# Performance work log

Hardware: AMD Instinct MI355X
Metric: run time of the kernel (lower is better)

## Reference

```python
import jax, jax.numpy as jnp
import numpy as np

N = 8192          # n_nodes; must equal OUT due to _weight_norm broadcasting
IN = 512          # in_features
OUT = 8192        # out_features
ALPHA = 0.2       # leaky relu negative slope
NEG_INF = -9e15   # mask value used by the torch module


def setup_inputs() -> dict:
    key = jax.random.key(0)
    k1, k2, k3, k4 = jax.random.split(key, 4)
    x = jax.random.normal(k1, (N, IN), jnp.float32)
    adj = jax.random.randint(k2, (N, N), 0, 2, jnp.int32)
    # nn.Linear weight [out_features, in_features]
    W = jax.random.normal(k3, (OUT, IN), jnp.float32) / np.sqrt(IN)
    # attention vector a: [2*out_features, 1], xavier_uniform-ish scale
    a = jax.random.normal(k4, (2 * OUT, 1), jnp.float32) * (1.414 * np.sqrt(2.0 / (2 * OUT + 1)))
    return {"x": x, "adj": adj, "W": W, "a": a}


def reference(x, adj, W, a):
    h = x @ W.T                                   # [N, OUT] (OUT == N)
    # torch._weight_norm(h, g, dim=1) = h * g / ||h||_cols  (norm over dim 0, kept as [1, OUT])
    col_norm = jnp.linalg.norm(h, axis=0, keepdims=True)   # [1, OUT]
    a1 = a[:OUT]                                  # [OUT, 1]
    a2 = a[OUT:]                                  # [OUT, 1]
    wn1 = h * (a1 / col_norm)                     # [N, N]: h[i,j]*a1[i]/norm[j]
    wn2 = h * (a2 / col_norm)                     # [N, N]
    e = jax.nn.leaky_relu(wn1 + wn2.T, ALPHA)     # [N, N]
    scores = jnp.where(adj > 0, e, NEG_INF)
    attention = jax.nn.softmax(scores, axis=1)    # dropout omitted (eval / deterministic)
    return attention @ h                          # [N, OUT]
```

## Files before the change

### kernel.cpp

```cpp
#include <hip/hip_runtime.h>
#include <hip/hip_bf16.h>
#include <stdint.h>

#define NN 8192
#define KIN 512

typedef __attribute__((ext_vector_type(8))) short bfx8;
typedef __attribute__((ext_vector_type(4))) float f32x4;
typedef __attribute__((ext_vector_type(4))) short sh4;

__device__ __forceinline__ float b2f(unsigned short u) {
  union { unsigned int i; float f; } z; z.i = ((unsigned int)u) << 16; return z.f;
}
__device__ __forceinline__ unsigned short f2b(float f) {
  __hip_bfloat16 h = __float2bfloat16(f);
  union { __hip_bfloat16 h; unsigned short u; } z; z.h = h; return z.u;
}

__device__ __forceinline__ void async16(void* lds, const void* g) {
  __builtin_amdgcn_global_load_lds(
      (const __attribute__((address_space(1))) unsigned int*)g,
      (__attribute__((address_space(3))) unsigned int*)lds,
      16, 0, 0);
}

__global__ __launch_bounds__(256)
void cvt_f32_bf16(const float* __restrict__ in, unsigned short* __restrict__ out, int n4) {
  int i = blockIdx.x * 256 + threadIdx.x;
  if (i >= n4) return;
  const float4 v = reinterpret_cast<const float4*>(in)[i];
  sh4 o;
  o.x = (short)f2b(v.x); o.y = (short)f2b(v.y);
  o.z = (short)f2b(v.z); o.w = (short)f2b(v.w);
  reinterpret_cast<sh4*>(out)[i] = o;
}

__global__ __launch_bounds__(256)
void transpose_cvt(const float* __restrict__ x, unsigned short* __restrict__ xT,
                   int NR, int NC) {
  __shared__ float t[64][65];
  const int i0 = blockIdx.x << 6;
  const int c0 = blockIdx.y << 6;
  const int tid = threadIdx.x;
  const int rl = tid >> 4;
  const int cl = (tid & 15) << 2;
#pragma unroll
  for (int ps = 0; ps < 4; ++ps) {
    const int r = rl + (ps << 4);
    const float4 v = *reinterpret_cast<const float4*>(&x[(size_t)(i0 + r) * NC + c0 + cl]);
    t[r][cl] = v.x; t[r][cl + 1] = v.y; t[r][cl + 2] = v.z; t[r][cl + 3] = v.w;
  }
  __syncthreads();
  const int cr = tid >> 3;
  const int il = (tid & 7) << 3;
#pragma unroll
  for (int ps = 0; ps < 2; ++ps) {
    const int c = cr + (ps << 5);
    bfx8 o;
#pragma unroll
    for (int j = 0; j < 8; ++j) o[j] = (short)f2b(t[il + j][c]);
    *reinterpret_cast<bfx8*>(&xT[(size_t)(c0 + c) * NR + i0 + il]) = o;
  }
}

template<int OUT_BF16>
__global__ __launch_bounds__(256)
void gemm_bt(const unsigned short* __restrict__ A,
             const unsigned short* __restrict__ B,
             void* __restrict__ C,
             const float* __restrict__ rowscale,
             int M, int Nc, int K)
{
  __shared__ unsigned short As[2][128 * 32];
  __shared__ unsigned short Bs[2][128 * 32];

  const int tid  = threadIdx.x;
  const int lane = tid & 63;
  const int wave = tid >> 6;
  const int wr   = wave >> 1, wc = wave & 1;

  const int nwg = gridDim.x;
  const int cpx = nwg >> 3;
  const int bid = blockIdx.x;
  const int swz = (bid & 7) * cpx + (bid >> 3);
  const int nbn = Nc >> 7;
  const int bm  = (swz / nbn) << 7;
  const int bn  = (swz % nbn) << 7;

  const int off0 = (wave << 10) + (lane << 4);
  const int r0   = off0 >> 6;
  const int k0e  = (off0 & 63) >> 1;
  const int r1   = r0 + 64;

  const unsigned short* Ag0 = A + (size_t)(bm + r0) * K + k0e;
  const unsigned short* Ag1 = A + (size_t)(bm + r1) * K + k0e;
  const unsigned short* Bg0 = B + (size_t)(bn + r0) * K + k0e;
  const unsigned short* Bg1 = B + (size_t)(bn + r1) * K + k0e;

  f32x4 acc[4][4];
#pragma unroll
  for (int m = 0; m < 4; ++m)
#pragma unroll
    for (int n = 0; n < 4; ++n)
      acc[m][n] = (f32x4){0.f, 0.f, 0.f, 0.f};

  const int ldsoff = (wave << 10);

  auto stage = [&](int buf, int kk) {
    char* la = (char*)&As[buf][0] + ldsoff;
    char* lb = (char*)&Bs[buf][0] + ldsoff;
    async16(la,        Ag0 + kk);
    async16(la + 4096, Ag1 + kk);
    async16(lb,        Bg0 + kk);
    async16(lb + 4096, Bg1 + kk);
  };

  stage(0, 0);
  __syncthreads();

  const int nk   = K >> 5;
  const int arow = (wr << 6) + (lane & 15);
  const int brow = (wc << 6) + (lane & 15);
  const int koff = (lane >> 4) << 3;

  for (int kt = 0; kt < nk; ++kt) {
    const int cur = kt & 1;
    if (kt + 1 < nk) stage(cur ^ 1, (kt + 1) << 5);

    bfx8 af[4], bf[4];
#pragma unroll
    for (int m = 0; m < 4; ++m)
      af[m] = *reinterpret_cast<const bfx8*>(&As[cur][(arow + (m << 4)) * 32 + koff]);
#pragma unroll
    for (int n = 0; n < 4; ++n)
      bf[n] = *reinterpret_cast<const bfx8*>(&Bs[cur][(brow + (n << 4)) * 32 + koff]);

#pragma unroll
    for (int m = 0; m < 4; ++m)
#pragma unroll
      for (int n = 0; n < 4; ++n)
        acc[m][n] = __builtin_amdgcn_mfma_f32_16x16x32_bf16(af[m], bf[n], acc[m][n], 0, 0, 0);

    __syncthreads();
  }

#pragma unroll
  for (int m = 0; m < 4; ++m) {
    const int rowb = bm + (wr << 6) + (m << 4) + ((lane >> 4) << 2);
#pragma unroll
    for (int j = 0; j < 4; ++j) {
      const int r = rowb + j;
      if (OUT_BF16) {
        unsigned short* Cb = (unsigned short*)C;
#pragma unroll
        for (int n = 0; n < 4; ++n)
          Cb[(size_t)r * Nc + bn + (wc << 6) + (n << 4) + (lane & 15)] = f2b(acc[m][n][j]);
      } else {
        const float s = rowscale[r];
        float* Cf = (float*)C;
#pragma unroll
        for (int n = 0; n < 4; ++n)
          Cf[(size_t)r * Nc + bn + (wc << 6) + (n << 4) + (lane & 15)] = acc[m][n][j] * s;
      }
    }
  }
}

template<int MODE>
__global__ __launch_bounds__(256)
void row_reduce(const unsigned short* __restrict__ X, float* __restrict__ out, int ncols) {
  const int row = blockIdx.x;
  const unsigned short* xr = X + (size_t)row * ncols;
  float s = 0.f;
  for (int c = threadIdx.x * 8; c < ncols; c += 2048) {
    bfx8 v = *reinterpret_cast<const bfx8*>(xr + c);
#pragma unroll
    for (int j = 0; j < 8; ++j) {
      float f = b2f((unsigned short)v[j]);
      s += (MODE == 0) ? f * f : f;
    }
  }
#pragma unroll
  for (int o = 32; o > 0; o >>= 1) s += __shfl_down(s, o);
  __shared__ float red[4];
  if ((threadIdx.x & 63) == 0) red[threadIdx.x >> 6] = s;
  __syncthreads();
  if (threadIdx.x == 0) {
    float t = red[0] + red[1] + red[2] + red[3];
    out[row] = (MODE == 0) ? (1.0f / sqrtf(t)) : (1.0f / t);
  }
}

__global__ __launch_bounds__(256)
void invert_vec(float* __restrict__ v) {
  const int i = blockIdx.x * 256 + threadIdx.x;
  v[i] = 1.0f / v[i];
}

__global__ __launch_bounds__(256)
void scores_kernel(const unsigned short* __restrict__ hT,
                   const int* __restrict__ adj,
                   const float* __restrict__ a,
                   const float* __restrict__ icn,
                   unsigned short* __restrict__ p,
                   float* __restrict__ rs_raw,
                   int strip)
{
  __shared__ unsigned short T1t[64][72];

  const int tid   = threadIdx.x;
  const int i0    = blockIdx.x << 6;
  const int jbase = blockIdx.y * strip;
  const int ntile = strip >> 6;

  const int slot = tid & 7;
  const int jb   = slot << 3;
  const int il0  = tid >> 3;
  const int i_p0 = i0 + il0;
  const int i_p1 = i_p0 + 32;
  const float a1_0 = a[i_p0], ici_0 = icn[i_p0];
  const float a1_1 = a[i_p1], ici_1 = icn[i_p1];
  float rs0 = 0.f, rs1 = 0.f;

  const int rblk0 = (((jb >> 3) ^ ((il0 >> 3) & 7)) << 3);
  const int rblk1 = (((jb >> 3) ^ (((il0 + 32) >> 3) & 7)) << 3);

  for (int jt = 0; jt < ntile; ++jt) {
    const int j0 = jbase + (jt << 6);
    __syncthreads();
#pragma unroll
    for (int ss = 0; ss < 2; ++ss) {
      const int u  = tid + (ss << 8);
      const int jr = u >> 3;
      const int cb = (u & 7) << 3;
      const bfx8 v = *reinterpret_cast<const bfx8*>(hT + (size_t)(j0 + jr) * NN + i0 + cb);
      const int colp = ((((jr >> 3) ^ (u & 7)) << 3) | (jr & 7));
#pragma unroll
      for (int k = 0; k < 8; ++k) T1t[cb + k][colp] = (unsigned short)v[k];
    }
    __syncthreads();

    const int j = j0 + jb;
    const float4 ic0 = *reinterpret_cast<const float4*>(icn + j);
    const float4 ic1 = *reinterpret_cast<const float4*>(icn + j + 4);
    const float4 a20 = *reinterpret_cast<const float4*>(a + NN + j);
    const float4 a21 = *reinterpret_cast<const float4*>(a + NN + j + 4);
    const float icj[8] = {ic0.x, ic0.y, ic0.z, ic0.w, ic1.x, ic1.y, ic1.z, ic1.w};
    const float a2j[8] = {a20.x, a20.y, a20.z, a20.w, a21.x, a21.y, a21.z, a21.w};

#pragma unroll
    for (int ps = 0; ps < 2; ++ps) {
      const int il   = (ps == 0) ? il0 : il0 + 32;
      const int i    = (ps == 0) ? i_p0 : i_p1;
      const float a1 = (ps == 0) ? a1_0 : a1_1;
      const float ii = (ps == 0) ? ici_0 : ici_1;
      const int rb   = (ps == 0) ? rblk0 : rblk1;

      const bfx8 hijv = *reinterpret_cast<const bfx8*>(&T1t[il][rb]);
      const bfx8 hjiv = *reinterpret_cast<const bfx8*>(hT + (size_t)i * NN + j);
      const int4 ad0  = *reinterpret_cast<const int4*>(adj + (size_t)i * NN + j);
      const int4 ad1  = *reinterpret_cast<const int4*>(adj + (size_t)i * NN + j + 4);
      const int adv[8] = {ad0.x, ad0.y, ad0.z, ad0.w, ad1.x, ad1.y, ad1.z, ad1.w};

      bfx8 o;
      float rs = 0.f;
#pragma unroll
      for (int k = 0; k < 8; ++k) {
        const float hij = b2f((unsigned short)hijv[k]);
        const float hji = b2f((unsigned short)hjiv[k]);
        const float e0  = hij * (a1 * icj[k]) + hji * (a2j[k] * ii);
        const float e   = e0 > 0.f ? e0 : 0.2f * e0;
        const float pv  = (adv[k] > 0) ? __expf(e) : 0.f;
        const unsigned short ub = f2b(pv);
        o[k] = (short)ub;
        rs += b2f(ub);
      }
      *reinterpret_cast<bfx8*>(p + (size_t)i * NN + j) = o;
      if (ps == 0) rs0 += rs; else rs1 += rs;
    }
  }

#pragma unroll
  for (int o = 1; o < 8; o <<= 1) {
    rs0 += __shfl_xor(rs0, o);
    rs1 += __shfl_xor(rs1, o);
  }
  if (slot == 0) {
    atomicAdd(rs_raw + i_p0, rs0);
    atomicAdd(rs_raw + i_p1, rs1);
  }
}

extern "C" void kernel_launch(void* const* d_in, const int* in_sizes, int n_in,
                              void* d_out, int out_size, void* d_ws, size_t ws_size,
                              hipStream_t stream)
{
  (void)in_sizes; (void)n_in; (void)out_size; (void)ws_size;
  const float* x   = (const float*)d_in[0];
  const int*   adj = (const int*)d_in[1];
  const float* W   = (const float*)d_in[2];
  const float* a   = (const float*)d_in[3];
  float* out = (float*)d_out;

  char* ws = (char*)d_ws;
  unsigned short* hT = (unsigned short*)ws;
  unsigned short* p  = (unsigned short*)(ws + 134217728ull);
  unsigned short* xb = p;
  unsigned short* Wb = p + (size_t)NN * KIN;
  unsigned short* Axb = hT;
  unsigned short* xT  = hT + (size_t)NN * KIN;
  unsigned short* Wb2 = hT + 2 * (size_t)NN * KIN;
  float* icn = (float*)(ws + 268435456ull);
  float* irs = (float*)(ws + 268435456ull + 32768ull);

  hipMemsetAsync(irs, 0, NN * sizeof(float), stream);

  const int n4 = NN * KIN / 4;
  cvt_f32_bf16<<<n4 / 256, 256, 0, stream>>>(x, xb, n4);
  cvt_f32_bf16<<<n4 / 256, 256, 0, stream>>>(W, Wb, n4);

  gemm_bt<1><<<4096, 256, 0, stream>>>(Wb, xb, hT, nullptr, NN, NN, KIN);

  row_reduce<0><<<NN, 256, 0, stream>>>(hT, icn, NN);

  scores_kernel<<<dim3(128, 16), 256, 0, stream>>>(hT, adj, a, icn, p, irs, NN / 16);

  invert_vec<<<NN / 256, 256, 0, stream>>>(irs);

  cvt_f32_bf16<<<n4 / 256, 256, 0, stream>>>(W, Wb2, n4);
  transpose_cvt<<<dim3(NN / 64, KIN / 64), 256, 0, stream>>>(x, xT, NN, KIN);

  gemm_bt<1><<<256, 256, 0, stream>>>(p, xT, Axb, nullptr, NN, KIN, NN);

  gemm_bt<0><<<4096, 256, 0, stream>>>(Axb, Wb2, out, irs, NN, NN, KIN);
}
```

Baseline: 594.7 us.

## Split-K the attention-times-x GEMM with fp32 partials and a reduction kernel

The p·xT GEMM previously launched only 256 workgroups, each looping over the full K=8192 dimension, which left the GPU underoccupied. It is now split eight ways along K into 2048 workgroups, each writing fp32 partials into the output buffer used as scratch. A new kernel sums the eight partial planes and converts the result to bf16 for the final GEMM. This adds extra memory traffic for the partials and one extra kernel launch.

```diff
diff --git a/kernel.cpp b/kernel.cpp
--- a/kernel.cpp
+++ b/kernel.cpp
@@ -36,6 +36,24 @@
 }
 
 __global__ __launch_bounds__(256)
+void reduce_cvt(const float* __restrict__ P, unsigned short* __restrict__ out, int n4) {
+  const int i = blockIdx.x * 256 + threadIdx.x;
+  if (i >= n4) return;
+  const size_t plane = (size_t)NN * KIN / 4;
+  const float4* P4 = reinterpret_cast<const float4*>(P);
+  float4 s = P4[i];
+#pragma unroll
+  for (int sp = 1; sp < 8; ++sp) {
+    const float4 v = P4[i + sp * plane];
+    s.x += v.x; s.y += v.y; s.z += v.z; s.w += v.w;
+  }
+  sh4 o;
+  o.x = (short)f2b(s.x); o.y = (short)f2b(s.y);
+  o.z = (short)f2b(s.z); o.w = (short)f2b(s.w);
+  reinterpret_cast<sh4*>(out)[i] = o;
+}
+
+__global__ __launch_bounds__(256)
 void transpose_cvt(const float* __restrict__ x, unsigned short* __restrict__ xT,
                    int NR, int NC) {
   __shared__ float t[64][65];
@@ -63,7 +81,7 @@
   }
 }
 
-template<int OUT_BF16>
+template<int MODE, int SPLITS>
 __global__ __launch_bounds__(256)
 void gemm_bt(const unsigned short* __restrict__ A,
              const unsigned short* __restrict__ B,
@@ -83,19 +101,24 @@
   const int cpx = nwg >> 3;
   const int bid = blockIdx.x;
   const int swz = (bid & 7) * cpx + (bid >> 3);
+  const int bps = nwg / SPLITS;
+  const int split = swz / bps;
+  const int rem   = swz % bps;
   const int nbn = Nc >> 7;
-  const int bm  = (swz / nbn) << 7;
-  const int bn  = (swz % nbn) << 7;
+  const int bm  = (rem / nbn) << 7;
+  const int bn  = (rem % nbn) << 7;
+  const int klen  = K / SPLITS;
+  const int kbase = split * klen;
 
   const int off0 = (wave << 10) + (lane << 4);
   const int r0   = off0 >> 6;
   const int k0e  = (off0 & 63) >> 1;
   const int r1   = r0 + 64;
 
-  const unsigned short* Ag0 = A + (size_t)(bm + r0) * K + k0e;
-  const unsigned short* Ag1 = A + (size_t)(bm + r1) * K + k0e;
-  const unsigned short* Bg0 = B + (size_t)(bn + r0) * K + k0e;
-  const unsigned short* Bg1 = B + (size_t)(bn + r1) * K + k0e;
+  const unsigned short* Ag0 = A + (size_t)(bm + r0) * K + kbase + k0e;
+  const unsigned short* Ag1 = A + (size_t)(bm + r1) * K + kbase + k0e;
+  const unsigned short* Bg0 = B + (size_t)(bn + r0) * K + kbase + k0e;
+  const unsigned short* Bg1 = B + (size_t)(bn + r1) * K + kbase + k0e;
 
   f32x4 acc[4][4];
 #pragma unroll
@@ -118,7 +141,7 @@
   stage(0, 0);
   __syncthreads();
 
-  const int nk   = K >> 5;
+  const int nk   = klen >> 5;
   const int arow = (wr << 6) + (lane & 15);
   const int brow = (wc << 6) + (lane & 15);
   const int koff = (lane >> 4) << 3;
@@ -150,17 +173,22 @@
 #pragma unroll
     for (int j = 0; j < 4; ++j) {
       const int r = rowb + j;
-      if (OUT_BF16) {
+      if (MODE == 1) {
         unsigned short* Cb = (unsigned short*)C;
 #pragma unroll
         for (int n = 0; n < 4; ++n)
           Cb[(size_t)r * Nc + bn + (wc << 6) + (n << 4) + (lane & 15)] = f2b(acc[m][n][j]);
-      } else {
+      } else if (MODE == 0) {
         const float s = rowscale[r];
         float* Cf = (float*)C;
 #pragma unroll
         for (int n = 0; n < 4; ++n)
           Cf[(size_t)r * Nc + bn + (wc << 6) + (n << 4) + (lane & 15)] = acc[m][n][j] * s;
+      } else {
+        float* Cf = (float*)C + (size_t)split * M * Nc;
+#pragma unroll
+        for (int n = 0; n < 4; ++n)
+          Cf[(size_t)r * Nc + bn + (wc << 6) + (n << 4) + (lane & 15)] = acc[m][n][j];
       }
     }
   }
@@ -312,6 +340,7 @@
   unsigned short* Wb2 = hT + 2 * (size_t)NN * KIN;
   float* icn = (float*)(ws + 268435456ull);
   float* irs = (float*)(ws + 268435456ull + 32768ull);
+  float* parts = out;
 
   hipMemsetAsync(irs, 0, NN * sizeof(float), stream);
 
@@ -319,7 +348,7 @@
   cvt_f32_bf16<<<n4 / 256, 256, 0, stream>>>(x, xb, n4);
   cvt_f32_bf16<<<n4 / 256, 256, 0, stream>>>(W, Wb, n4);
 
-  gemm_bt<1><<<4096, 256, 0, stream>>>(Wb, xb, hT, nullptr, NN, NN, KIN);
+  gemm_bt<1, 1><<<4096, 256, 0, stream>>>(Wb, xb, hT, nullptr, NN, NN, KIN);
 
   row_reduce<0><<<NN, 256, 0, stream>>>(hT, icn, NN);
 
@@ -330,7 +359,9 @@
   cvt_f32_bf16<<<n4 / 256, 256, 0, stream>>>(W, Wb2, n4);
   transpose_cvt<<<dim3(NN / 64, KIN / 64), 256, 0, stream>>>(x, xT, NN, KIN);
 
-  gemm_bt<1><<<256, 256, 0, stream>>>(p, xT, Axb, nullptr, NN, KIN, NN);
-
-  gemm_bt<0><<<4096, 256, 0, stream>>>(Axb, Wb2, out, irs, NN, NN, KIN);
-}
+  gemm_bt<2, 8><<<2048, 256, 0, stream>>>(p, xT, parts, nullptr, NN, KIN, NN);
+
+  reduce_cvt<<<n4 / 256, 256, 0, stream>>>(parts, Axb, n4);
+
+  gemm_bt<0, 1><<<4096, 256, 0, stream>>>(Axb, Wb2, out, irs, NN, NN, KIN);
+}
```

Result: faster. 545.7 us (-8.2%).
